# Optimization experiments

Hardware: AMD Instinct MI355X
Metric: run time of the kernel (lower is better)

The kernel has to match this reference:

```python
import jax, jax.numpy as jnp
import numpy as np

NUM_NODES = 100000
NUM_EDGES = 1000000
NUM_REL = 3
NUM_GRAPHS = 512
VOCAB = 10000
EMBED_DIM = 64
HIDDEN_DIM = 64
NUM_CLS = 2


def setup_inputs() -> dict:
    key = jax.random.key(0)
    ks = jax.random.split(key, 10)
    x = jax.random.randint(ks[0], (NUM_NODES,), 0, VOCAB)
    edge_index = jax.random.randint(ks[1], (2, NUM_EDGES), 0, NUM_NODES)
    edge_type = jax.random.randint(ks[2], (NUM_EDGES,), 0, NUM_REL)
    batch = jnp.sort(jax.random.randint(ks[3], (NUM_NODES,), 0, NUM_GRAPHS))
    embed_table = jax.random.normal(ks[4], (VOCAB, EMBED_DIM), dtype=jnp.float32) * 0.02
    embed_table = embed_table.at[0].set(0.0)  # padding_idx=0
    W_rel = jax.random.normal(ks[5], (NUM_REL, EMBED_DIM, HIDDEN_DIM), dtype=jnp.float32) * 0.1
    W_root = jax.random.normal(ks[6], (EMBED_DIM, HIDDEN_DIM), dtype=jnp.float32) * 0.1
    conv_bias = jax.random.normal(ks[7], (HIDDEN_DIM,), dtype=jnp.float32) * 0.01
    lin_W = jax.random.normal(ks[8], (HIDDEN_DIM, NUM_CLS), dtype=jnp.float32) * 0.1
    lin_b = jnp.zeros((NUM_CLS,), dtype=jnp.float32)
    return {"x": x, "edge_index": edge_index, "edge_type": edge_type, "batch": batch,
            "embed_table": embed_table, "W_rel": W_rel, "W_root": W_root,
            "conv_bias": conv_bias, "lin_W": lin_W, "lin_b": lin_b}


def reference(x, edge_index, edge_type, batch, embed_table, W_rel, W_root, conv_bias, lin_W, lin_b):
    # Embedding lookup (padding row already zeroed)
    h = embed_table[x]                                   # [N, D]
    src, dst = edge_index[0], edge_index[1]
    # RGCNConv: root transform + per-relation mean-aggregated neighbor transform
    out = h @ W_root + conv_bias                          # [N, H]
    for r in range(NUM_REL):
        mask = (edge_type == r).astype(h.dtype)           # [E]
        hr = h @ W_rel[r]                                 # [N, H] tiny GEMM
        msg = hr[src] * mask[:, None]                     # [E, H] gather
        agg = jax.ops.segment_sum(msg, dst, num_segments=NUM_NODES)
        cnt = jax.ops.segment_sum(mask, dst, num_segments=NUM_NODES)
        out = out + agg / jnp.maximum(cnt, 1.0)[:, None]
    out = jax.nn.relu(out)
    # global_mean_pool over graph ids
    g_sum = jax.ops.segment_sum(out, batch, num_segments=NUM_GRAPHS)    # [G, H]
    g_cnt = jax.ops.segment_sum(jnp.ones_like(batch, dtype=out.dtype), batch, num_segments=NUM_GRAPHS)
    g_emb = g_sum / jnp.maximum(g_cnt, 1.0)[:, None]
    return g_emb @ lin_W + lin_b                          # [G, num_cls]
```

## Files before the change

### kernel.cpp

```cpp
#include <hip/hip_runtime.h>

#define N_NODES 100000
#define N_EDGES 1000000
#define N_GRAPHS 512
#define VOCAB 10000
#define DIM 64

#define NPB 64
#define NB 1563
#define EPB 4096
#define SB 245
#define NELEMS (NB * SB)
#define BUILD_BLOCKS ((4 * VOCAB) / 16)
#define CAP 1152

typedef unsigned short ushort_t;

static __device__ __forceinline__ ushort_t f2bf(float f) {
    unsigned u = __float_as_uint(f);
    unsigned r = 0x7FFFu + ((u >> 16) & 1u);
    return (ushort_t)((u + r) >> 16);
}
#define BFLO(u) __uint_as_float((u) << 16)
#define BFHI(u) __uint_as_float((u) & 0xFFFF0000u)

__global__ __launch_bounds__(256)
void hist_build(const int* __restrict__ dst, int* __restrict__ bh,
                float* __restrict__ g_sum,
                const float* __restrict__ embed,
                const float* __restrict__ W_rel,
                const float* __restrict__ W_root,
                ushort_t* __restrict__ Tb) {
    if (blockIdx.x < SB) {
        for (int i = blockIdx.x * 256 + threadIdx.x; i < N_GRAPHS * DIM; i += SB * 256)
            g_sum[i] = 0.f;
        __shared__ int h[NB];
        for (int i = threadIdx.x; i < NB; i += 256) h[i] = 0;
        __syncthreads();
        int base = blockIdx.x * EPB;
        int lim  = base + EPB; if (lim > N_EDGES) lim = N_EDGES;
        for (int e = base + threadIdx.x; e < lim; e += 256)
            atomicAdd(&h[dst[e] >> 6], 1);
        __syncthreads();
        for (int i = threadIdx.x; i < NB; i += 256)
            bh[i * SB + blockIdx.x] = h[i];
    } else {
        int tid  = (blockIdx.x - SB) * 256 + threadIdx.x;
        int l    = tid & 63;
        int wave = tid >> 6;
        int sub  = l >> 4;
        int q    = l & 15;
        int row  = wave * 4 + sub;
        int m    = row / VOCAB;
        int v    = row - m * VOCAB;
        const float* W = (m == 0) ? W_root : (W_rel + (size_t)(m - 1) * DIM * DIM);
        float4 e4  = *(const float4*)(embed + (size_t)v * DIM + q * 4);
        float4 acc = {0.f, 0.f, 0.f, 0.f};
#pragma unroll
        for (int kk = 0; kk < 16; ++kk) {
            int srcl = sub * 16 + kk;
            float ex = __shfl(e4.x, srcl, 64);
            float ey = __shfl(e4.y, srcl, 64);
            float ez = __shfl(e4.z, srcl, 64);
            float ew = __shfl(e4.w, srcl, 64);
            const float4 w0 = *(const float4*)(W + (4 * kk + 0) * DIM + q * 4);
            const float4 w1 = *(const float4*)(W + (4 * kk + 1) * DIM + q * 4);
            const float4 w2 = *(const float4*)(W + (4 * kk + 2) * DIM + q * 4);
            const float4 w3 = *(const float4*)(W + (4 * kk + 3) * DIM + q * 4);
            acc.x += ex * w0.x; acc.y += ex * w0.y; acc.z += ex * w0.z; acc.w += ex * w0.w;
            acc.x += ey * w1.x; acc.y += ey * w1.y; acc.z += ey * w1.z; acc.w += ey * w1.w;
            acc.x += ez * w2.x; acc.y += ez * w2.y; acc.z += ez * w2.z; acc.w += ez * w2.w;
            acc.x += ew * w3.x; acc.y += ew * w3.y; acc.z += ew * w3.z; acc.w += ew * w3.w;
        }
        ushort_t* p = Tb + (size_t)row * DIM + q * 4;
        p[0] = f2bf(acc.x); p[1] = f2bf(acc.y);
        p[2] = f2bf(acc.z); p[3] = f2bf(acc.w);
    }
}

__global__ __launch_bounds__(256)
void rowscan(const int* __restrict__ bh, int* __restrict__ loc,
             int* __restrict__ btot) {
    __shared__ int wsum4[4];
    int b = blockIdx.x, t = threadIdx.x;
    int l = t & 63, wv = t >> 6;
    int v = (t < SB) ? bh[b * SB + t] : 0;
    int sc = v;
#pragma unroll
    for (int d = 1; d < 64; d <<= 1) {
        int tt = __shfl_up(sc, d, 64);
        if (l >= d) sc += tt;
    }
    if (l == 63) wsum4[wv] = sc;
    __syncthreads();
    if (t == 0) {
        int a = 0;
#pragma unroll
        for (int k = 0; k < 4; ++k) { int tmp = wsum4[k]; wsum4[k] = a; a += tmp; }
    }
    __syncthreads();
    int excl = sc - v + wsum4[wv];
    if (t < SB) loc[b * SB + t] = excl;
    if (t == 255) btot[b] = excl;
}

__global__ __launch_bounds__(1024)
void gscan(const int* __restrict__ btot, int* __restrict__ bbase) {
    __shared__ int wsum[16];
    int t = threadIdx.x;
    int i0 = 2 * t, i1 = 2 * t + 1;
    int a = (i0 < NB) ? btot[i0] : 0;
    int c = (i1 < NB) ? btot[i1] : 0;
    int pv = a + c;
    int l = t & 63, wv = t >> 6;
    int sc = pv;
#pragma unroll
    for (int d = 1; d < 64; d <<= 1) {
        int tt = __shfl_up(sc, d, 64);
        if (l >= d) sc += tt;
    }
    if (l == 63) wsum[wv] = sc;
    __syncthreads();
    if (wv == 0) {
        int wval = (l < 16) ? wsum[l] : 0;
        int ss = wval;
#pragma unroll
        for (int d = 1; d < 16; d <<= 1) {
            int tt = __shfl_up(ss, d, 64);
            if (l >= d) ss += tt;
        }
        if (l < 16) wsum[l] = ss - wval;
    }
    __syncthreads();
    int E = sc - pv + wsum[wv];
    if (i0 <= NB) bbase[i0] = E;
    if (i1 <= NB) bbase[i1] = E + a;
}

__global__ __launch_bounds__(512)
void bucket_scatter(const int* __restrict__ src,
                    const int* __restrict__ dst,
                    const int* __restrict__ etype,
                    const int* __restrict__ x,
                    const int* __restrict__ loc,
                    const int* __restrict__ bbase,
                    unsigned* __restrict__ rec) {
    __shared__ int baseh[NB];
    __shared__ int h[NB];
    for (int i = threadIdx.x; i < NB; i += 512) {
        baseh[i] = bbase[i] + loc[i * SB + blockIdx.x];
        h[i] = 0;
    }
    __syncthreads();
    int base = blockIdx.x * EPB;
    int lim  = base + EPB; if (lim > N_EDGES) lim = N_EDGES;
    for (int e = base + threadIdx.x; e < lim; e += 512) {
        int d = dst[e];
        int b = d >> 6;
        int rk = atomicAdd(&h[b], 1);
        unsigned payload = ((unsigned)x[src[e]] << 8)
                         | ((unsigned)(d & 63) << 2)
                         | (unsigned)etype[e];
        rec[baseh[b] + rk] = payload;
    }
}

__global__ __launch_bounds__(256)
void sort_aggregate(const int* __restrict__ x,
                    const int* __restrict__ batch,
                    const int* __restrict__ bbase,
                    const unsigned* __restrict__ rec,
                    const ushort_t* __restrict__ Tb,
                    const float* __restrict__ bias,
                    float* __restrict__ g_sum) {
    __shared__ int cstart[257];
    __shared__ int cur[256];
    __shared__ int wsum4[4];
    __shared__ float inv_sh[256];
    __shared__ unsigned sortedc[CAP];
    __shared__ float rows[NPB * DIM];
    __shared__ float red[256];
    __shared__ int batch_sh[NPB];
    int b = blockIdx.x, t = threadIdx.x;
    int s = bbase[b];
    int e = bbase[b + 1];
    int ne = e - s;
    int nvalid = N_NODES - b * NPB; if (nvalid > NPB) nvalid = NPB;

    cstart[t] = 0;
    if (t < NPB) batch_sh[t] = (t < nvalid) ? batch[b * NPB + t] : -1;
    __syncthreads();
    for (int i = t; i < ne; i += 256)
        atomicAdd(&cstart[rec[s + i] & 0xFFu], 1);
    __syncthreads();
    {
        int l = t & 63, wv = t >> 6;
        int v = cstart[t];
        int sc = v;
#pragma unroll
        for (int d = 1; d < 64; d <<= 1) {
            int tt = __shfl_up(sc, d, 64);
            if (l >= d) sc += tt;
        }
        if (l == 63) wsum4[wv] = sc;
        __syncthreads();
        if (t == 0) {
            int a = 0;
#pragma unroll
            for (int k = 0; k < 4; ++k) { int tmp = wsum4[k]; wsum4[k] = a; a += tmp; }
        }
        __syncthreads();
        int excl = sc - v + wsum4[wv];
        __syncthreads();
        cstart[t] = excl;
        cur[t] = excl;
        if (t == 255) cstart[256] = excl + v;
    }
    __syncthreads();
    inv_sh[t] = 1.f / fmaxf((float)(cstart[t + 1] - cstart[t]), 1.f);
    for (int i = t; i < ne; i += 256) {
        unsigned p = rec[s + i];
        int rk = atomicAdd(&cur[p & 0xFFu], 1);
        sortedc[rk] = p;
    }
    __syncthreads();

    int grp = t >> 3;
    int sl  = t & 7;
    const ushort_t* TbRel = Tb + (size_t)VOCAB * DIM;
#pragma unroll
    for (int nn = 0; nn < 2; ++nn) {
        int n = grp * 2 + nn;
        if (n >= nvalid) continue;
        int node = b * NPB + n;
        int i0 = cstart[n << 2];
        int i1 = cstart[(n + 1) << 2];
        float a0 = 0.f, a1 = 0.f, a2 = 0.f, a3 = 0.f,
              a4 = 0.f, a5 = 0.f, a6 = 0.f, a7 = 0.f;
        int i = i0;
        for (; i + 2 <= i1; i += 2) {
            unsigned c1 = sortedc[i], c2 = sortedc[i + 1];
            const uint4 t1 = *(const uint4*)(TbRel +
                ((size_t)(c1 & 3u) * VOCAB + (c1 >> 8)) * DIM + sl * 8);
            const uint4 t2 = *(const uint4*)(TbRel +
                ((size_t)(c2 & 3u) * VOCAB + (c2 >> 8)) * DIM + sl * 8);
            float iv1 = inv_sh[c1 & 0xFFu];
            float iv2 = inv_sh[c2 & 0xFFu];
            a0 += BFLO(t1.x) * iv1; a1 += BFHI(t1.x) * iv1;
            a2 += BFLO(t1.y) * iv1; a3 += BFHI(t1.y) * iv1;
            a4 += BFLO(t1.z) * iv1; a5 += BFHI(t1.z) * iv1;
            a6 += BFLO(t1.w) * iv1; a7 += BFHI(t1.w) * iv1;
            a0 += BFLO(t2.x) * iv2; a1 += BFHI(t2.x) * iv2;
            a2 += BFLO(t2.y) * iv2; a3 += BFHI(t2.y) * iv2;
            a4 += BFLO(t2.z) * iv2; a5 += BFHI(t2.z) * iv2;
            a6 += BFLO(t2.w) * iv2; a7 += BFHI(t2.w) * iv2;
        }
        if (i < i1) {
            unsigned c1 = sortedc[i];
            const uint4 t1 = *(const uint4*)(TbRel +
                ((size_t)(c1 & 3u) * VOCAB + (c1 >> 8)) * DIM + sl * 8);
            float iv1 = inv_sh[c1 & 0xFFu];
            a0 += BFLO(t1.x) * iv1; a1 += BFHI(t1.x) * iv1;
            a2 += BFLO(t1.y) * iv1; a3 += BFHI(t1.y) * iv1;
            a4 += BFLO(t1.z) * iv1; a5 += BFHI(t1.z) * iv1;
            a6 += BFLO(t1.w) * iv1; a7 += BFHI(t1.w) * iv1;
        }
        int xv = x[node];
        const uint4 rt = *(const uint4*)(Tb + (size_t)xv * DIM + sl * 8);
        const float4 b0 = *(const float4*)(bias + sl * 8);
        const float4 b1 = *(const float4*)(bias + sl * 8 + 4);
        float* rp = rows + n * DIM + sl * 8;
        rp[0] = fmaxf(BFLO(rt.x) + b0.x + a0, 0.f);
        rp[1] = fmaxf(BFHI(rt.x) + b0.y + a1, 0.f);
        rp[2] = fmaxf(BFLO(rt.y) + b0.z + a2, 0.f);
        rp[3] = fmaxf(BFHI(rt.y) + b0.w + a3, 0.f);
        rp[4] = fmaxf(BFLO(rt.z) + b1.x + a4, 0.f);
        rp[5] = fmaxf(BFHI(rt.z) + b1.y + a5, 0.f);
        rp[6] = fmaxf(BFLO(rt.w) + b1.z + a6, 0.f);
        rp[7] = fmaxf(BFHI(rt.w) + b1.w + a7, 0.f);
    }
    __syncthreads();

    int gmin = batch_sh[0];
    int gmax = batch_sh[nvalid - 1];
    int f  = t & 63;
    int n0 = t >> 6;
    for (int g = gmin; g <= gmax; ++g) {
        float a = 0.f;
        for (int n = n0; n < nvalid; n += 4)
            a += (batch_sh[n] == g) ? rows[n * DIM + f] : 0.f;
        red[t] = a;
        __syncthreads();
        if (t < 64) {
            float tot = red[t] + red[t + 64] + red[t + 128] + red[t + 192];
            if (tot != 0.f) atomicAdd(&g_sum[g * DIM + t], tot);
        }
        __syncthreads();
    }
}

__device__ __forceinline__ int lbound(const int* __restrict__ b, int val) {
    int lo = 0, hi = N_NODES;
    while (lo < hi) {
        int mid = (lo + hi) >> 1;
        if (b[mid] < val) lo = mid + 1; else hi = mid;
    }
    return lo;
}

__global__ __launch_bounds__(64)
void final_linear(const int* __restrict__ batch,
                  const float* __restrict__ g_sum,
                  const float* __restrict__ lin_W,
                  const float* __restrict__ lin_b,
                  float* __restrict__ out) {
    int g = blockIdx.x;
    int l = threadIdx.x;
    int s = lbound(batch, g);
    int e = lbound(batch, g + 1);
    float mean = (e > s) ? g_sum[g * DIM + l] / (float)(e - s) : 0.f;
    float p0 = mean * lin_W[l * 2 + 0];
    float p1 = mean * lin_W[l * 2 + 1];
#pragma unroll
    for (int off2 = 32; off2 > 0; off2 >>= 1) {
        p0 += __shfl_down(p0, off2, 64);
        p1 += __shfl_down(p1, off2, 64);
    }
    if (l == 0) {
        out[g * 2 + 0] = p0 + lin_b[0];
        out[g * 2 + 1] = p1 + lin_b[1];
    }
}

extern "C" void kernel_launch(void* const* d_in, const int* in_sizes, int n_in,
                              void* d_out, int out_size, void* d_ws, size_t ws_size,
                              hipStream_t stream) {
    const int*   x      = (const int*)d_in[0];
    const int*   eidx   = (const int*)d_in[1];
    const int*   etype  = (const int*)d_in[2];
    const int*   batch  = (const int*)d_in[3];
    const float* embed  = (const float*)d_in[4];
    const float* W_rel  = (const float*)d_in[5];
    const float* W_root = (const float*)d_in[6];
    const float* bias   = (const float*)d_in[7];
    const float* lin_W  = (const float*)d_in[8];
    const float* lin_b  = (const float*)d_in[9];
    float* out = (float*)d_out;

    const int* src = eidx;
    const int* dst = eidx + N_EDGES;

    char* ws = (char*)d_ws;
    ushort_t* Tb    = (ushort_t*)(ws);
    unsigned* rec   = (unsigned*)(ws + 5120000);
    int* loc        = (int*)(ws + 9120000);
    int* btot       = (int*)(ws + 10651776);
    int* bbase      = (int*)(ws + 10658048);
    int* bh         = (int*)(ws + 10664320);
    float* g_sum    = (float*)(ws + 12196096);

    hist_build<<<SB + BUILD_BLOCKS, 256, 0, stream>>>(
        dst, bh, g_sum, embed, W_rel, W_root, Tb);

    rowscan<<<NB, 256, 0, stream>>>(bh, loc, btot);

    gscan<<<1, 1024, 0, stream>>>(btot, bbase);

    bucket_scatter<<<SB, 512, 0, stream>>>(src, dst, etype, x, loc, bbase, rec);

    sort_aggregate<<<NB, 256, 0, stream>>>(x, batch, bbase, rec, Tb, bias, g_sum);

    final_linear<<<N_GRAPHS, 64, 0, stream>>>(batch, g_sum, lin_W, lin_b, out);
}
```

Baseline: 87.46 us.

## Fold global scan into rowscan via last-block pattern and enlarge edge chunks

```diff
diff --git a/kernel.cpp b/kernel.cpp
--- a/kernel.cpp
+++ b/kernel.cpp
@@ -8,10 +8,9 @@
 
 #define NPB 64
 #define NB 1563
-#define EPB 4096
-#define SB 245
-#define NELEMS (NB * SB)
-#define BUILD_BLOCKS ((4 * VOCAB) / 16)
+#define EPB 8192
+#define SB 123
+#define BUILD_BLOCKS ((4 * VOCAB) / 64)
 #define CAP 1152
 
 typedef unsigned short ushort_t;
@@ -24,28 +23,29 @@
 #define BFLO(u) __uint_as_float((u) << 16)
 #define BFHI(u) __uint_as_float((u) & 0xFFFF0000u)
 
-__global__ __launch_bounds__(256)
+__global__ __launch_bounds__(1024)
 void hist_build(const int* __restrict__ dst, int* __restrict__ bh,
-                float* __restrict__ g_sum,
+                float* __restrict__ g_sum, int* __restrict__ done,
                 const float* __restrict__ embed,
                 const float* __restrict__ W_rel,
                 const float* __restrict__ W_root,
                 ushort_t* __restrict__ Tb) {
     if (blockIdx.x < SB) {
-        for (int i = blockIdx.x * 256 + threadIdx.x; i < N_GRAPHS * DIM; i += SB * 256)
+        for (int i = blockIdx.x * 1024 + threadIdx.x; i < N_GRAPHS * DIM; i += SB * 1024)
             g_sum[i] = 0.f;
+        if (blockIdx.x == 0 && threadIdx.x == 0) *done = 0;
         __shared__ int h[NB];
-        for (int i = threadIdx.x; i < NB; i += 256) h[i] = 0;
+        for (int i = threadIdx.x; i < NB; i += 1024) h[i] = 0;
         __syncthreads();
         int base = blockIdx.x * EPB;
         int lim  = base + EPB; if (lim > N_EDGES) lim = N_EDGES;
-        for (int e = base + threadIdx.x; e < lim; e += 256)
+        for (int e = base + threadIdx.x; e < lim; e += 1024)
             atomicAdd(&h[dst[e] >> 6], 1);
         __syncthreads();
-        for (int i = threadIdx.x; i < NB; i += 256)
+        for (int i = threadIdx.x; i < NB; i += 1024)
             bh[i * SB + blockIdx.x] = h[i];
     } else {
-        int tid  = (blockIdx.x - SB) * 256 + threadIdx.x;
+        int tid  = (blockIdx.x - SB) * 1024 + threadIdx.x;
         int l    = tid & 63;
         int wave = tid >> 6;
         int sub  = l >> 4;
@@ -80,8 +80,10 @@
 
 __global__ __launch_bounds__(256)
 void rowscan(const int* __restrict__ bh, int* __restrict__ loc,
-             int* __restrict__ btot) {
+             int* __restrict__ btot, int* __restrict__ done,
+             int* __restrict__ bbase) {
     __shared__ int wsum4[4];
+    __shared__ int isLast;
     int b = blockIdx.x, t = threadIdx.x;
     int l = t & 63, wv = t >> 6;
     int v = (t < SB) ? bh[b * SB + t] : 0;
@@ -102,42 +104,43 @@
     int excl = sc - v + wsum4[wv];
     if (t < SB) loc[b * SB + t] = excl;
     if (t == 255) btot[b] = excl;
+
+    __threadfence();
+    if (t == 0) isLast = (atomicAdd(done, 1) == NB - 1);
+    __syncthreads();
+    if (!isLast) return;
+    __syncthreads();
+    int base = t * 8;
+    int vals[8];
+    int lsum = 0;
+#pragma unroll
+    for (int k = 0; k < 8; ++k) {
+        vals[k] = (base + k < NB) ? btot[base + k] : 0;
+        lsum += vals[k];
+    }
+    int sc2 = lsum;
+#pragma unroll
+    for (int d = 1; d < 64; d <<= 1) {
+        int tt = __shfl_up(sc2, d, 64);
+        if (l >= d) sc2 += tt;
+    }
+    if (l == 63) wsum4[wv] = sc2;
+    __syncthreads();
+    if (t == 0) {
+        int a = 0;
+#pragma unroll
+        for (int k = 0; k < 4; ++k) { int tmp = wsum4[k]; wsum4[k] = a; a += tmp; }
+    }
+    __syncthreads();
+    int run = sc2 - lsum + wsum4[wv];
+#pragma unroll
+    for (int k = 0; k < 8; ++k) {
+        if (base + k <= NB) bbase[base + k] = run;
+        run += vals[k];
+    }
 }
 
 __global__ __launch_bounds__(1024)
-void gscan(const int* __restrict__ btot, int* __restrict__ bbase) {
-    __shared__ int wsum[16];
-    int t = threadIdx.x;
-    int i0 = 2 * t, i1 = 2 * t + 1;
-    int a = (i0 < NB) ? btot[i0] : 0;
-    int c = (i1 < NB) ? btot[i1] : 0;
-    int pv = a + c;
-    int l = t & 63, wv = t >> 6;
-    int sc = pv;
-#pragma unroll
-    for (int d = 1; d < 64; d <<= 1) {
-        int tt = __shfl_up(sc, d, 64);
-        if (l >= d) sc += tt;
-    }
-    if (l == 63) wsum[wv] = sc;
-    __syncthreads();
-    if (wv == 0) {
-        int wval = (l < 16) ? wsum[l] : 0;
-        int ss = wval;
-#pragma unroll
-        for (int d = 1; d < 16; d <<= 1) {
-            int tt = __shfl_up(ss, d, 64);
-            if (l >= d) ss += tt;
-        }
-        if (l < 16) wsum[l] = ss - wval;
-    }
-    __syncthreads();
-    int E = sc - pv + wsum[wv];
-    if (i0 <= NB) bbase[i0] = E;
-    if (i1 <= NB) bbase[i1] = E + a;
-}
-
-__global__ __launch_bounds__(512)
 void bucket_scatter(const int* __restrict__ src,
                     const int* __restrict__ dst,
                     const int* __restrict__ etype,
@@ -147,14 +150,14 @@
                     unsigned* __restrict__ rec) {
     __shared__ int baseh[NB];
     __shared__ int h[NB];
-    for (int i = threadIdx.x; i < NB; i += 512) {
+    for (int i = threadIdx.x; i < NB; i += 1024) {
         baseh[i] = bbase[i] + loc[i * SB + blockIdx.x];
         h[i] = 0;
     }
     __syncthreads();
     int base = blockIdx.x * EPB;
     int lim  = base + EPB; if (lim > N_EDGES) lim = N_EDGES;
-    for (int e = base + threadIdx.x; e < lim; e += 512) {
+    for (int e = base + threadIdx.x; e < lim; e += 1024) {
         int d = dst[e];
         int b = d >> 6;
         int rk = atomicAdd(&h[b], 1);
@@ -238,14 +241,19 @@
         float a0 = 0.f, a1 = 0.f, a2 = 0.f, a3 = 0.f,
               a4 = 0.f, a5 = 0.f, a6 = 0.f, a7 = 0.f;
         int i = i0;
-        for (; i + 2 <= i1; i += 2) {
-            unsigned c1 = sortedc[i], c2 = sortedc[i + 1];
+        for (; i + 4 <= i1; i += 4) {
+            unsigned c1 = sortedc[i],     c2 = sortedc[i + 1];
+            unsigned c3 = sortedc[i + 2], c4 = sortedc[i + 3];
             const uint4 t1 = *(const uint4*)(TbRel +
                 ((size_t)(c1 & 3u) * VOCAB + (c1 >> 8)) * DIM + sl * 8);
             const uint4 t2 = *(const uint4*)(TbRel +
                 ((size_t)(c2 & 3u) * VOCAB + (c2 >> 8)) * DIM + sl * 8);
-            float iv1 = inv_sh[c1 & 0xFFu];
-            float iv2 = inv_sh[c2 & 0xFFu];
+            const uint4 t3 = *(const uint4*)(TbRel +
+                ((size_t)(c3 & 3u) * VOCAB + (c3 >> 8)) * DIM + sl * 8);
+            const uint4 t4 = *(const uint4*)(TbRel +
+                ((size_t)(c4 & 3u) * VOCAB + (c4 >> 8)) * DIM + sl * 8);
+            float iv1 = inv_sh[c1 & 0xFFu], iv2 = inv_sh[c2 & 0xFFu];
+            float iv3 = inv_sh[c3 & 0xFFu], iv4 = inv_sh[c4 & 0xFFu];
             a0 += BFLO(t1.x) * iv1; a1 += BFHI(t1.x) * iv1;
             a2 += BFLO(t1.y) * iv1; a3 += BFHI(t1.y) * iv1;
             a4 += BFLO(t1.z) * iv1; a5 += BFHI(t1.z) * iv1;
@@ -254,8 +262,16 @@
             a2 += BFLO(t2.y) * iv2; a3 += BFHI(t2.y) * iv2;
             a4 += BFLO(t2.z) * iv2; a5 += BFHI(t2.z) * iv2;
             a6 += BFLO(t2.w) * iv2; a7 += BFHI(t2.w) * iv2;
-        }
-        if (i < i1) {
+            a0 += BFLO(t3.x) * iv3; a1 += BFHI(t3.x) * iv3;
+            a2 += BFLO(t3.y) * iv3; a3 += BFHI(t3.y) * iv3;
+            a4 += BFLO(t3.z) * iv3; a5 += BFHI(t3.z) * iv3;
+            a6 += BFLO(t3.w) * iv3; a7 += BFHI(t3.w) * iv3;
+            a0 += BFLO(t4.x) * iv4; a1 += BFHI(t4.x) * iv4;
+            a2 += BFLO(t4.y) * iv4; a3 += BFHI(t4.y) * iv4;
+            a4 += BFLO(t4.z) * iv4; a5 += BFHI(t4.z) * iv4;
+            a6 += BFLO(t4.w) * iv4; a7 += BFHI(t4.w) * iv4;
+        }
+        for (; i < i1; ++i) {
             unsigned c1 = sortedc[i];
             const uint4 t1 = *(const uint4*)(TbRel +
                 ((size_t)(c1 & 3u) * VOCAB + (c1 >> 8)) * DIM + sl * 8);
@@ -354,19 +370,18 @@
     ushort_t* Tb    = (ushort_t*)(ws);
     unsigned* rec   = (unsigned*)(ws + 5120000);
     int* loc        = (int*)(ws + 9120000);
-    int* btot       = (int*)(ws + 10651776);
-    int* bbase      = (int*)(ws + 10658048);
-    int* bh         = (int*)(ws + 10664320);
-    float* g_sum    = (float*)(ws + 12196096);
-
-    hist_build<<<SB + BUILD_BLOCKS, 256, 0, stream>>>(
-        dst, bh, g_sum, embed, W_rel, W_root, Tb);
-
-    rowscan<<<NB, 256, 0, stream>>>(bh, loc, btot);
-
-    gscan<<<1, 1024, 0, stream>>>(btot, bbase);
-
-    bucket_scatter<<<SB, 512, 0, stream>>>(src, dst, etype, x, loc, bbase, rec);
+    int* btot       = (int*)(ws + 9889024);
+    int* bbase      = (int*)(ws + 9895296);
+    int* bh         = (int*)(ws + 9901568);
+    float* g_sum    = (float*)(ws + 10670592);
+    int* done       = (int*)(ws + 10801664);
+
+    hist_build<<<SB + BUILD_BLOCKS, 1024, 0, stream>>>(
+        dst, bh, g_sum, done, embed, W_rel, W_root, Tb);
+
+    rowscan<<<NB, 256, 0, stream>>>(bh, loc, btot, done, bbase);
+
+    bucket_scatter<<<SB, 1024, 0, stream>>>(src, dst, etype, x, loc, bbase, rec);
 
     sort_aggregate<<<NB, 256, 0, stream>>>(x, batch, bbase, rec, Tb, bias, g_sum);
 
```

Result: slower. 190.7 us (+118.0%).

## Fold global bucket scan into bucket_scatter, transpose histogram layout, unroll gather by four

Applied to the files above, without the earlier changes.

```diff
diff --git a/kernel.cpp b/kernel.cpp
--- a/kernel.cpp
+++ b/kernel.cpp
@@ -10,7 +10,6 @@
 #define NB 1563
 #define EPB 4096
 #define SB 245
-#define NELEMS (NB * SB)
 #define BUILD_BLOCKS ((4 * VOCAB) / 16)
 #define CAP 1152
 
@@ -43,7 +42,7 @@
             atomicAdd(&h[dst[e] >> 6], 1);
         __syncthreads();
         for (int i = threadIdx.x; i < NB; i += 256)
-            bh[i * SB + blockIdx.x] = h[i];
+            bh[blockIdx.x * NB + i] = h[i];
     } else {
         int tid  = (blockIdx.x - SB) * 256 + threadIdx.x;
         int l    = tid & 63;
@@ -84,7 +83,7 @@
     __shared__ int wsum4[4];
     int b = blockIdx.x, t = threadIdx.x;
     int l = t & 63, wv = t >> 6;
-    int v = (t < SB) ? bh[b * SB + t] : 0;
+    int v = (t < SB) ? bh[t * NB + b] : 0;
     int sc = v;
 #pragma unroll
     for (int d = 1; d < 64; d <<= 1) {
@@ -102,39 +101,6 @@
     int excl = sc - v + wsum4[wv];
     if (t < SB) loc[b * SB + t] = excl;
     if (t == 255) btot[b] = excl;
-}
-
-__global__ __launch_bounds__(1024)
-void gscan(const int* __restrict__ btot, int* __restrict__ bbase) {
-    __shared__ int wsum[16];
-    int t = threadIdx.x;
-    int i0 = 2 * t, i1 = 2 * t + 1;
-    int a = (i0 < NB) ? btot[i0] : 0;
-    int c = (i1 < NB) ? btot[i1] : 0;
-    int pv = a + c;
-    int l = t & 63, wv = t >> 6;
-    int sc = pv;
-#pragma unroll
-    for (int d = 1; d < 64; d <<= 1) {
-        int tt = __shfl_up(sc, d, 64);
-        if (l >= d) sc += tt;
-    }
-    if (l == 63) wsum[wv] = sc;
-    __syncthreads();
-    if (wv == 0) {
-        int wval = (l < 16) ? wsum[l] : 0;
-        int ss = wval;
-#pragma unroll
-        for (int d = 1; d < 16; d <<= 1) {
-            int tt = __shfl_up(ss, d, 64);
-            if (l >= d) ss += tt;
-        }
-        if (l < 16) wsum[l] = ss - wval;
-    }
-    __syncthreads();
-    int E = sc - pv + wsum[wv];
-    if (i0 <= NB) bbase[i0] = E;
-    if (i1 <= NB) bbase[i1] = E + a;
 }
 
 __global__ __launch_bounds__(512)
@@ -143,18 +109,54 @@
                     const int* __restrict__ etype,
                     const int* __restrict__ x,
                     const int* __restrict__ loc,
-                    const int* __restrict__ bbase,
+                    const int* __restrict__ btot,
+                    int* __restrict__ bbase,
                     unsigned* __restrict__ rec) {
+    __shared__ int wsum8[8];
     __shared__ int baseh[NB];
     __shared__ int h[NB];
-    for (int i = threadIdx.x; i < NB; i += 512) {
-        baseh[i] = bbase[i] + loc[i * SB + blockIdx.x];
+    int t = threadIdx.x;
+    int l = t & 63, wv = t >> 6;
+
+    int v0 = (4 * t + 0 < NB) ? btot[4 * t + 0] : 0;
+    int v1 = (4 * t + 1 < NB) ? btot[4 * t + 1] : 0;
+    int v2 = (4 * t + 2 < NB) ? btot[4 * t + 2] : 0;
+    int v3 = (4 * t + 3 < NB) ? btot[4 * t + 3] : 0;
+    int lsum = v0 + v1 + v2 + v3;
+    int sc = lsum;
+#pragma unroll
+    for (int d = 1; d < 64; d <<= 1) {
+        int tt = __shfl_up(sc, d, 64);
+        if (l >= d) sc += tt;
+    }
+    if (l == 63) wsum8[wv] = sc;
+    __syncthreads();
+    if (t == 0) {
+        int a = 0;
+#pragma unroll
+        for (int k = 0; k < 8; ++k) { int tmp = wsum8[k]; wsum8[k] = a; a += tmp; }
+    }
+    __syncthreads();
+    int p = sc - lsum + wsum8[wv];
+    if (4 * t + 0 < NB) baseh[4 * t + 0] = p; p += v0;
+    if (4 * t + 1 < NB) baseh[4 * t + 1] = p; p += v1;
+    if (4 * t + 2 < NB) baseh[4 * t + 2] = p; p += v2;
+    if (4 * t + 3 < NB) baseh[4 * t + 3] = p;
+    __syncthreads();
+
+    if (blockIdx.x == 0) {
+        for (int i = t; i < NB; i += 512) bbase[i] = baseh[i];
+        if (t == 0) bbase[NB] = N_EDGES;
+    }
+    for (int i = t; i < NB; i += 512) {
+        baseh[i] += loc[i * SB + blockIdx.x];
         h[i] = 0;
     }
     __syncthreads();
+
     int base = blockIdx.x * EPB;
     int lim  = base + EPB; if (lim > N_EDGES) lim = N_EDGES;
-    for (int e = base + threadIdx.x; e < lim; e += 512) {
+    for (int e = base + t; e < lim; e += 512) {
         int d = dst[e];
         int b = d >> 6;
         int rk = atomicAdd(&h[b], 1);
@@ -238,14 +240,19 @@
         float a0 = 0.f, a1 = 0.f, a2 = 0.f, a3 = 0.f,
               a4 = 0.f, a5 = 0.f, a6 = 0.f, a7 = 0.f;
         int i = i0;
-        for (; i + 2 <= i1; i += 2) {
-            unsigned c1 = sortedc[i], c2 = sortedc[i + 1];
+        for (; i + 4 <= i1; i += 4) {
+            unsigned c1 = sortedc[i],     c2 = sortedc[i + 1];
+            unsigned c3 = sortedc[i + 2], c4 = sortedc[i + 3];
             const uint4 t1 = *(const uint4*)(TbRel +
                 ((size_t)(c1 & 3u) * VOCAB + (c1 >> 8)) * DIM + sl * 8);
             const uint4 t2 = *(const uint4*)(TbRel +
                 ((size_t)(c2 & 3u) * VOCAB + (c2 >> 8)) * DIM + sl * 8);
-            float iv1 = inv_sh[c1 & 0xFFu];
-            float iv2 = inv_sh[c2 & 0xFFu];
+            const uint4 t3 = *(const uint4*)(TbRel +
+                ((size_t)(c3 & 3u) * VOCAB + (c3 >> 8)) * DIM + sl * 8);
+            const uint4 t4 = *(const uint4*)(TbRel +
+                ((size_t)(c4 & 3u) * VOCAB + (c4 >> 8)) * DIM + sl * 8);
+            float iv1 = inv_sh[c1 & 0xFFu], iv2 = inv_sh[c2 & 0xFFu];
+            float iv3 = inv_sh[c3 & 0xFFu], iv4 = inv_sh[c4 & 0xFFu];
             a0 += BFLO(t1.x) * iv1; a1 += BFHI(t1.x) * iv1;
             a2 += BFLO(t1.y) * iv1; a3 += BFHI(t1.y) * iv1;
             a4 += BFLO(t1.z) * iv1; a5 += BFHI(t1.z) * iv1;
@@ -254,8 +261,16 @@
             a2 += BFLO(t2.y) * iv2; a3 += BFHI(t2.y) * iv2;
             a4 += BFLO(t2.z) * iv2; a5 += BFHI(t2.z) * iv2;
             a6 += BFLO(t2.w) * iv2; a7 += BFHI(t2.w) * iv2;
-        }
-        if (i < i1) {
+            a0 += BFLO(t3.x) * iv3; a1 += BFHI(t3.x) * iv3;
+            a2 += BFLO(t3.y) * iv3; a3 += BFHI(t3.y) * iv3;
+            a4 += BFLO(t3.z) * iv3; a5 += BFHI(t3.z) * iv3;
+            a6 += BFLO(t3.w) * iv3; a7 += BFHI(t3.w) * iv3;
+            a0 += BFLO(t4.x) * iv4; a1 += BFHI(t4.x) * iv4;
+            a2 += BFLO(t4.y) * iv4; a3 += BFHI(t4.y) * iv4;
+            a4 += BFLO(t4.z) * iv4; a5 += BFHI(t4.z) * iv4;
+            a6 += BFLO(t4.w) * iv4; a7 += BFHI(t4.w) * iv4;
+        }
+        for (; i < i1; ++i) {
             unsigned c1 = sortedc[i];
             const uint4 t1 = *(const uint4*)(TbRel +
                 ((size_t)(c1 & 3u) * VOCAB + (c1 >> 8)) * DIM + sl * 8);
@@ -364,9 +379,7 @@
 
     rowscan<<<NB, 256, 0, stream>>>(bh, loc, btot);
 
-    gscan<<<1, 1024, 0, stream>>>(btot, bbase);
-
-    bucket_scatter<<<SB, 512, 0, stream>>>(src, dst, etype, x, loc, bbase, rec);
+    bucket_scatter<<<SB, 512, 0, stream>>>(src, dst, etype, x, loc, btot, bbase, rec);
 
     sort_aggregate<<<NB, 256, 0, stream>>>(x, batch, bbase, rec, Tb, bias, g_sum);
 
```

After: 84.80 us. 1.03x faster.
